# Kernel tuning notes

Hardware: AMD Instinct MI355X
Metric: run time of the kernel (lower is better)

Reference implementation:

```python
import jax, jax.numpy as jnp
import numpy as np

N, D = 8192, 128
BATCH_SIZE = 8192  # init kwarg; final loss divisor
EPS = 1e-12        # F.normalize eps


def _normalize(x):
    n = jnp.maximum(jnp.linalg.norm(x, axis=-1, keepdims=True), EPS)
    return x / n


def _alignment(x, y, alpha=2.0):
    # (x - y).norm(p=2, dim=1).pow(2).mean() == mean of squared row diffs
    return jnp.mean(jnp.sum((x - y) ** 2, axis=1))


def _uniformity(x, t=2.0):
    # torch.pdist(x).pow(2) == squared euclidean distance for all i<j pairs.
    # Use gram-matrix identity; mask to strict upper triangle.
    n = x.shape[0]
    sq = jnp.sum(x * x, axis=1)                      # [N]
    d2 = sq[:, None] + sq[None, :] - 2.0 * (x @ x.T)  # [N, N]
    d2 = jnp.maximum(d2, 0.0)
    iu = jnp.triu(jnp.ones((n, n), dtype=bool), k=1)
    num_pairs = n * (n - 1) // 2
    mean_val = jnp.sum(jnp.where(iu, jnp.exp(-t * d2), 0.0)) / num_pairs
    return jnp.log(mean_val)


def setup_inputs() -> dict:
    key = jax.random.key(0)
    k1, k2, k3 = jax.random.split(key, 3)
    return {
        "users": jax.random.normal(k1, (N, D), dtype=jnp.float32),
        "pos_items": jax.random.normal(k2, (N, D), dtype=jnp.float32),
        "neg_items": jax.random.normal(k3, (N, D), dtype=jnp.float32),
    }


def reference(users, pos_items, neg_items):
    # neg_items is accepted but unused, matching the original forward.
    user_n = _normalize(users)
    item_n = _normalize(pos_items)
    align = _alignment(user_n, item_n)
    uniform = 0.5 * (_uniformity(user_n) + _uniformity(item_n)) / 2.0
    loss = (align + uniform) / BATCH_SIZE
    return loss
```

## Files before the change

kernel.cpp:

```cpp
#include <hip/hip_runtime.h>
#include <hip/hip_bf16.h>

typedef int   i32x4  __attribute__((ext_vector_type(4)));
typedef int   i32x16 __attribute__((ext_vector_type(16)));

#define NROWS 8192
#define DIM   128
#define NB    64
#define JOBS_PER_MAT 2080

__device__ __forceinline__ float waveReduceSum(float v) {
    for (int off = 32; off; off >>= 1) v += __shfl_xor(v, off, 64);
    return v;
}

__device__ __forceinline__ float fast_exp2(float x) {
    return __builtin_amdgcn_exp2f(x);
}

__device__ __forceinline__ void gload16(const void* g, void* l) {
    __builtin_amdgcn_global_load_lds(
        (const __attribute__((address_space(1))) unsigned int*)(uintptr_t)g,
        (__attribute__((address_space(3))) unsigned int*)(uintptr_t)l,
        16, 0, 0);
}

__device__ __forceinline__ int tri(int b) { return b * NB - (b * (b - 1)) / 2; }

__global__ __launch_bounds__(256) void prep_kernel(
    const float* __restrict__ users, const float* __restrict__ pos,
    signed char* __restrict__ U8, signed char* __restrict__ P8,
    double* __restrict__ alignPart)
{
    const int tid  = threadIdx.x;
    const int lane = tid & 63;
    const int w    = tid >> 6;
    const int l32  = lane & 31;
    const int half = lane >> 5;
    const int r    = blockIdx.x * 8 + w * 2 + half;

    const float4 u4 = ((const float4*)users)[r * 32 + l32];
    const float4 p4 = ((const float4*)pos )[r * 32 + l32];

    float su = u4.x*u4.x + u4.y*u4.y + u4.z*u4.z + u4.w*u4.w;
    float sp = p4.x*p4.x + p4.y*p4.y + p4.z*p4.z + p4.w*p4.w;
    for (int off = 16; off; off >>= 1) {
        su += __shfl_xor(su, off, 64);
        sp += __shfl_xor(sp, off, 64);
    }
    const float nu  = fmaxf(sqrtf(su), 1e-12f);
    const float npp = fmaxf(sqrtf(sp), 1e-12f);

    const float ux = u4.x / nu,  uy = u4.y / nu,  uz = u4.z / nu,  uw = u4.w / nu;
    const float px = p4.x / npp, py = p4.y / npp, pz = p4.z / npp, pw = p4.w / npp;

    union { signed char c[4]; int i; } qu, qp;
    qu.c[0] = (signed char)__float2int_rn(ux * 127.0f);
    qu.c[1] = (signed char)__float2int_rn(uy * 127.0f);
    qu.c[2] = (signed char)__float2int_rn(uz * 127.0f);
    qu.c[3] = (signed char)__float2int_rn(uw * 127.0f);
    qp.c[0] = (signed char)__float2int_rn(px * 127.0f);
    qp.c[1] = (signed char)__float2int_rn(py * 127.0f);
    qp.c[2] = (signed char)__float2int_rn(pz * 127.0f);
    qp.c[3] = (signed char)__float2int_rn(pw * 127.0f);
    ((int*)U8)[r * 32 + l32] = qu.i;
    ((int*)P8)[r * 32 + l32] = qp.i;

    const float dx = ux - px, dy = uy - py, dz = uz - pz, dw = uw - pw;
    float al = dx*dx + dy*dy + dz*dz + dw*dw;
    for (int off = 16; off; off >>= 1) al += __shfl_xor(al, off, 64);
    al += __shfl_xor(al, 32, 64);

    __shared__ float wsum[4];
    if (lane == 0) wsum[w] = al;
    __syncthreads();
    if (tid == 0)
        alignPart[blockIdx.x] = (double)wsum[0] + (double)wsum[1]
                              + (double)wsum[2] + (double)wsum[3];
}

__global__ __launch_bounds__(256, 4) void gram_kernel(
    const signed char* __restrict__ U8, const signed char* __restrict__ P8,
    double* __restrict__ Spart)
{
    __shared__ __align__(16) unsigned char smem[32768];
    __shared__ float wsum[2][4];

    const int blk = blockIdx.x;
    const int j0  = blk * 2;
    const int mat = j0 >= JOBS_PER_MAT;
    const int t0  = j0 - (mat ? JOBS_PER_MAT : 0);

    int bi = (int)((NB + 0.5f) - sqrtf((NB + 0.5f) * (NB + 0.5f) - 2.0f * (float)t0));
    if (bi > 0 && tri(bi) > t0) --bi;
    if (tri(bi + 1) <= t0) ++bi;
    int bj = bi + (t0 - tri(bi));
    int bi1 = bi, bj1 = bj + 1;
    if (bj == NB - 1) { bi1 = bi + 1; bj1 = bi1; }

    const char* __restrict__ Xb = (const char*)(mat ? P8 : U8);

    const int tid  = threadIdx.x;
    const int lane = tid & 63;
    const int w    = tid >> 6;

    const int rl = lane >> 2;
    const int cg = (((lane & 3) ^ (rl & 3)) << 4);
    unsigned char* lbase = smem + w * 1024;

#define STAGE(p, h, tbi, tbj)                                               \
    {                                                                       \
        _Pragma("unroll")                                                   \
        for (int i_ = 0; i_ < 2; ++i_) {                                    \
            const int r_ = w * 16 + i_ * 64 + rl;                           \
            gload16(Xb + (size_t)((tbi) * 128 + r_) * 128 + (h) * 64 + cg,  \
                    lbase + (p) * 16384 + i_ * 4096);                       \
            gload16(Xb + (size_t)((tbj) * 128 + r_) * 128 + (h) * 64 + cg,  \
                    lbase + (p) * 16384 + 8192 + i_ * 4096);                \
        }                                                                   \
    }

    const int wm = w >> 1, wn = w & 1;
    const int l32 = lane & 31;
    const int lh  = lane >> 5;
    const unsigned cxor = (unsigned)(l32 & 3);
    const unsigned aRow0 = (unsigned)(wm * 64 + l32);
    const unsigned bRow0 = (unsigned)(wn * 64 + l32);

    i32x16 acc[2][2];
#define ZEROACC                                                             \
    _Pragma("unroll")                                                       \
    for (int mi_ = 0; mi_ < 2; ++mi_)                                       \
        _Pragma("unroll")                                                   \
        for (int ni_ = 0; ni_ < 2; ++ni_)                                   \
            _Pragma("unroll")                                               \
            for (int e_ = 0; e_ < 16; ++e_)                                 \
                acc[mi_][ni_][e_] = 0;
    ZEROACC

#define COMPUTE(p)                                                          \
    {                                                                       \
        const unsigned base = (p) * 16384;                                  \
        _Pragma("unroll")                                                   \
        for (int ks2 = 0; ks2 < 2; ++ks2) {                                 \
            const unsigned c = (((unsigned)(ks2 * 2 + lh)) ^ cxor) << 4;    \
            i32x4 a[2], b[2];                                               \
            _Pragma("unroll")                                               \
            for (int mi = 0; mi < 2; ++mi)                                  \
                a[mi] = *reinterpret_cast<const i32x4*>(                    \
                    smem + base + (aRow0 + mi * 32) * 64 + c);              \
            _Pragma("unroll")                                               \
            for (int ni = 0; ni < 2; ++ni)                                  \
                b[ni] = *reinterpret_cast<const i32x4*>(                    \
                    smem + base + 8192 + (bRow0 + ni * 32) * 64 + c);       \
            _Pragma("unroll")                                               \
            for (int mi = 0; mi < 2; ++mi)                                  \
                _Pragma("unroll")                                           \
                for (int ni = 0; ni < 2; ++ni)                              \
                    acc[mi][ni] = __builtin_amdgcn_mfma_i32_32x32x32_i8(    \
                        a[mi], b[ni], acc[mi][ni], 0, 0, 0);                \
        }                                                                   \
    }

    const float C1  = 4.0f * 1.4426950408889634f;
    const float C1s = C1 / 16129.0f;

#define EPILOGUE(slot)                                                      \
    {                                                                       \
        float s0 = 0.f, s1 = 0.f, s2 = 0.f, s3 = 0.f;                       \
        _Pragma("unroll")                                                   \
        for (int mi = 0; mi < 2; ++mi)                                      \
            _Pragma("unroll")                                               \
            for (int ni = 0; ni < 2; ++ni) {                                \
                const i32x16 v = acc[mi][ni];                               \
                _Pragma("unroll")                                           \
                for (int e = 0; e < 16; e += 4) {                           \
                    s0 += fast_exp2(fmaf((float)v[e + 0], C1s, -C1));       \
                    s1 += fast_exp2(fmaf((float)v[e + 1], C1s, -C1));       \
                    s2 += fast_exp2(fmaf((float)v[e + 2], C1s, -C1));       \
                    s3 += fast_exp2(fmaf((float)v[e + 3], C1s, -C1));       \
                }                                                           \
            }                                                               \
        const float s_ = waveReduceSum((s0 + s1) + (s2 + s3));              \
        if (lane == 0) wsum[slot][w] = s_;                                  \
    }

    STAGE(0, 0, bi, bj)
    __syncthreads();
    STAGE(1, 1, bi, bj)
    COMPUTE(0)
    __syncthreads();
    STAGE(0, 0, bi1, bj1)
    COMPUTE(1)
    EPILOGUE(0)
    ZEROACC
    __syncthreads();
    STAGE(1, 1, bi1, bj1)
    COMPUTE(0)
    if (tid == 0) {
        double bs = (double)wsum[0][0] + (double)wsum[0][1]
                  + (double)wsum[0][2] + (double)wsum[0][3];
        if (bi != bj) bs *= 2.0;
        Spart[j0] = bs;
    }
    __syncthreads();
    COMPUTE(1)
    EPILOGUE(1)
    __syncthreads();
    if (tid == 0) {
        double bs = (double)wsum[1][0] + (double)wsum[1][1]
                  + (double)wsum[1][2] + (double)wsum[1][3];
        if (bi1 != bj1) bs *= 2.0;
        Spart[j0 + 1] = bs;
    }
#undef STAGE
#undef COMPUTE
#undef ZEROACC
#undef EPILOGUE
}

__global__ __launch_bounds__(1024) void finalize_kernel(
    const double* __restrict__ alignPart, const double* __restrict__ Spart,
    float* __restrict__ out)
{
    const int tid = threadIdx.x;
    double a = 0.0, su = 0.0, sp = 0.0;
    for (int i = tid; i < 1024; i += 1024) a += alignPart[i];
    for (int i = tid; i < 2 * JOBS_PER_MAT; i += 1024) {
        const double v = Spart[i];
        if (i < JOBS_PER_MAT) su += v; else sp += v;
    }
    for (int off = 32; off; off >>= 1) {
        a  += __shfl_xor(a,  off, 64);
        su += __shfl_xor(su, off, 64);
        sp += __shfl_xor(sp, off, 64);
    }
    __shared__ double sh[3][16];
    const int lane = tid & 63, wid = tid >> 6;
    if (lane == 0) { sh[0][wid] = a; sh[1][wid] = su; sh[2][wid] = sp; }
    __syncthreads();
    if (tid == 0) {
        double A = 0.0, SU = 0.0, SP = 0.0;
        for (int i = 0; i < 16; ++i) { A += sh[0][i]; SU += sh[1][i]; SP += sh[2][i]; }
        const double Nd = 8192.0;
        const double npairs = Nd * (Nd - 1.0) * 0.5;
        const double align = A / Nd;
        const double mu = (SU - Nd) * 0.5 / npairs;
        const double mp = (SP - Nd) * 0.5 / npairs;
        const double uniform = 0.25 * (log(mu) + log(mp));
        out[0] = (float)((align + uniform) / 8192.0);
    }
}

extern "C" void kernel_launch(void* const* d_in, const int* in_sizes, int n_in,
                              void* d_out, int out_size, void* d_ws, size_t ws_size,
                              hipStream_t stream)
{
    const float* users = (const float*)d_in[0];
    const float* pos   = (const float*)d_in[1];
    float* out = (float*)d_out;

    char* ws = (char*)d_ws;
    signed char* U8 = (signed char*)ws;
    signed char* P8 = (signed char*)(ws + 1048576);
    double* alignPart = (double*)(ws + 2097152);
    double* Spart     = (double*)(ws + 2097152 + 8192);

    hipLaunchKernelGGL(prep_kernel, dim3(1024), dim3(256), 0, stream,
                       users, pos, U8, P8, alignPart);
    hipLaunchKernelGGL(gram_kernel, dim3(JOBS_PER_MAT), dim3(256), 0, stream,
                       U8, P8, Spart);
    hipLaunchKernelGGL(finalize_kernel, dim3(1), dim3(1024), 0, stream,
                       alignPart, Spart, out);
}
```

Before: 35.14 us.

## Process four gram tiles per block with full-K staging and double accumulators

Each gram block now handles four 128x128 tiles instead of two, staging the full 128-byte K dimension per tile into a 64KB double buffer rather than two 64-byte halves. Two accumulator sets alternate, so the exp epilogue of one tile overlaps the MFMA work of the next. The LDS swizzle widens to 8 chunks to match the 128-byte rows. The goal is fewer barriers and blocks and less per-tile epilogue exposure, paid for with double the shared memory, lower occupancy (launch bound 2) and more accumulator registers.

```diff
diff --git a/kernel.cpp b/kernel.cpp
--- a/kernel.cpp
+++ b/kernel.cpp
@@ -8,6 +8,7 @@
 #define DIM   128
 #define NB    64
 #define JOBS_PER_MAT 2080
+#define BLKS_PER_MAT 520
 
 __device__ __forceinline__ float waveReduceSum(float v) {
     for (int off = 32; off; off >>= 1) v += __shfl_xor(v, off, 64);
@@ -79,24 +80,29 @@
                               + (double)wsum[2] + (double)wsum[3];
 }
 
-__global__ __launch_bounds__(256, 4) void gram_kernel(
+__global__ __launch_bounds__(256, 2) void gram_kernel(
     const signed char* __restrict__ U8, const signed char* __restrict__ P8,
     double* __restrict__ Spart)
 {
-    __shared__ __align__(16) unsigned char smem[32768];
-    __shared__ float wsum[2][4];
+    __shared__ __align__(16) unsigned char smem[65536];
+    __shared__ float wsum[4][4];
 
     const int blk = blockIdx.x;
-    const int j0  = blk * 2;
-    const int mat = j0 >= JOBS_PER_MAT;
-    const int t0  = j0 - (mat ? JOBS_PER_MAT : 0);
+    const int mat = blk >= BLKS_PER_MAT;
+    const int t0  = (blk - (mat ? BLKS_PER_MAT : 0)) * 4;
 
     int bi = (int)((NB + 0.5f) - sqrtf((NB + 0.5f) * (NB + 0.5f) - 2.0f * (float)t0));
     if (bi > 0 && tri(bi) > t0) --bi;
     if (tri(bi + 1) <= t0) ++bi;
     int bj = bi + (t0 - tri(bi));
-    int bi1 = bi, bj1 = bj + 1;
-    if (bj == NB - 1) { bi1 = bi + 1; bj1 = bi1; }
+
+    int bis0 = bi, bjs0 = bj;
+    if (bj == NB - 1) { ++bi; bj = bi; } else ++bj;
+    int bis1 = bi, bjs1 = bj;
+    if (bj == NB - 1) { ++bi; bj = bi; } else ++bj;
+    int bis2 = bi, bjs2 = bj;
+    if (bj == NB - 1) { ++bi; bj = bi; } else ++bj;
+    int bis3 = bi, bjs3 = bj;
 
     const char* __restrict__ Xb = (const char*)(mat ? P8 : U8);
 
@@ -104,75 +110,74 @@
     const int lane = tid & 63;
     const int w    = tid >> 6;
 
-    const int rl = lane >> 2;
-    const int cg = (((lane & 3) ^ (rl & 3)) << 4);
-    unsigned char* lbase = smem + w * 1024;
-
-#define STAGE(p, h, tbi, tbj)                                               \
+    const int srow  = tid >> 3;
+    const int gcOff = (((tid & 7) ^ (srow & 7)) << 4);
+    unsigned char* lA0 = smem + w * 1024;
+
+#define STAGE(p, tbi, tbj)                                                  \
     {                                                                       \
         _Pragma("unroll")                                                   \
-        for (int i_ = 0; i_ < 2; ++i_) {                                    \
-            const int r_ = w * 16 + i_ * 64 + rl;                           \
-            gload16(Xb + (size_t)((tbi) * 128 + r_) * 128 + (h) * 64 + cg,  \
-                    lbase + (p) * 16384 + i_ * 4096);                       \
-            gload16(Xb + (size_t)((tbj) * 128 + r_) * 128 + (h) * 64 + cg,  \
-                    lbase + (p) * 16384 + 8192 + i_ * 4096);                \
+        for (int i_ = 0; i_ < 4; ++i_) {                                    \
+            gload16(Xb + (size_t)((tbi) * 128 + srow + 32 * i_) * 128 + gcOff, \
+                    lA0 + (p) * 32768 + i_ * 4096);                         \
+            gload16(Xb + (size_t)((tbj) * 128 + srow + 32 * i_) * 128 + gcOff, \
+                    lA0 + (p) * 32768 + 16384 + i_ * 4096);                 \
         }                                                                   \
     }
 
     const int wm = w >> 1, wn = w & 1;
     const int l32 = lane & 31;
     const int lh  = lane >> 5;
-    const unsigned cxor = (unsigned)(l32 & 3);
+    const unsigned cxor = (unsigned)(l32 & 7);
     const unsigned aRow0 = (unsigned)(wm * 64 + l32);
     const unsigned bRow0 = (unsigned)(wn * 64 + l32);
 
-    i32x16 acc[2][2];
-#define ZEROACC                                                             \
+    i32x16 accA[2][2], accB[2][2];
+
+#define ZERO(ACC)                                                           \
     _Pragma("unroll")                                                       \
     for (int mi_ = 0; mi_ < 2; ++mi_)                                       \
         _Pragma("unroll")                                                   \
         for (int ni_ = 0; ni_ < 2; ++ni_)                                   \
             _Pragma("unroll")                                               \
             for (int e_ = 0; e_ < 16; ++e_)                                 \
-                acc[mi_][ni_][e_] = 0;
-    ZEROACC
-
-#define COMPUTE(p)                                                          \
+                ACC[mi_][ni_][e_] = 0;
+
+#define COMPUTE(p, ACC)                                                     \
     {                                                                       \
-        const unsigned base = (p) * 16384;                                  \
-        _Pragma("unroll")                                                   \
-        for (int ks2 = 0; ks2 < 2; ++ks2) {                                 \
-            const unsigned c = (((unsigned)(ks2 * 2 + lh)) ^ cxor) << 4;    \
+        const unsigned base = (p) * 32768;                                  \
+        _Pragma("unroll")                                                   \
+        for (int ks = 0; ks < 4; ++ks) {                                    \
+            const unsigned c = (((unsigned)(ks * 2 + lh)) ^ cxor) << 4;     \
             i32x4 a[2], b[2];                                               \
             _Pragma("unroll")                                               \
             for (int mi = 0; mi < 2; ++mi)                                  \
                 a[mi] = *reinterpret_cast<const i32x4*>(                    \
-                    smem + base + (aRow0 + mi * 32) * 64 + c);              \
+                    smem + base + (aRow0 + mi * 32) * 128 + c);             \
             _Pragma("unroll")                                               \
             for (int ni = 0; ni < 2; ++ni)                                  \
                 b[ni] = *reinterpret_cast<const i32x4*>(                    \
-                    smem + base + 8192 + (bRow0 + ni * 32) * 64 + c);       \
+                    smem + base + 16384 + (bRow0 + ni * 32) * 128 + c);     \
             _Pragma("unroll")                                               \
             for (int mi = 0; mi < 2; ++mi)                                  \
                 _Pragma("unroll")                                           \
                 for (int ni = 0; ni < 2; ++ni)                              \
-                    acc[mi][ni] = __builtin_amdgcn_mfma_i32_32x32x32_i8(    \
-                        a[mi], b[ni], acc[mi][ni], 0, 0, 0);                \
+                    ACC[mi][ni] = __builtin_amdgcn_mfma_i32_32x32x32_i8(    \
+                        a[mi], b[ni], ACC[mi][ni], 0, 0, 0);                \
         }                                                                   \
     }
 
     const float C1  = 4.0f * 1.4426950408889634f;
     const float C1s = C1 / 16129.0f;
 
-#define EPILOGUE(slot)                                                      \
+#define EPI(ACC, slot)                                                      \
     {                                                                       \
         float s0 = 0.f, s1 = 0.f, s2 = 0.f, s3 = 0.f;                       \
         _Pragma("unroll")                                                   \
         for (int mi = 0; mi < 2; ++mi)                                      \
             _Pragma("unroll")                                               \
             for (int ni = 0; ni < 2; ++ni) {                                \
-                const i32x16 v = acc[mi][ni];                               \
+                const i32x16 v = ACC[mi][ni];                               \
                 _Pragma("unroll")                                           \
                 for (int e = 0; e < 16; e += 4) {                           \
                     s0 += fast_exp2(fmaf((float)v[e + 0], C1s, -C1));       \
@@ -185,38 +190,53 @@
         if (lane == 0) wsum[slot][w] = s_;                                  \
     }
 
-    STAGE(0, 0, bi, bj)
-    __syncthreads();
-    STAGE(1, 1, bi, bj)
-    COMPUTE(0)
-    __syncthreads();
-    STAGE(0, 0, bi1, bj1)
-    COMPUTE(1)
-    EPILOGUE(0)
-    ZEROACC
-    __syncthreads();
-    STAGE(1, 1, bi1, bj1)
-    COMPUTE(0)
+    ZERO(accA); ZERO(accB);
+    STAGE(0, bis0, bjs0)
+    __syncthreads();
+
+    STAGE(1, bis1, bjs1)
+    COMPUTE(0, accA)
+    __syncthreads();
+
+    STAGE(0, bis2, bjs2)
+    COMPUTE(1, accB)
+    EPI(accA, 0)
+    ZERO(accA);
+    __syncthreads();
+
+    STAGE(1, bis3, bjs3)
+    COMPUTE(0, accA)
+    EPI(accB, 1)
+    ZERO(accB);
+    __syncthreads();
+
+    COMPUTE(1, accB)
+    EPI(accA, 2)
+    EPI(accB, 3)
+    __syncthreads();
+
     if (tid == 0) {
-        double bs = (double)wsum[0][0] + (double)wsum[0][1]
+        double b0 = (double)wsum[0][0] + (double)wsum[0][1]
                   + (double)wsum[0][2] + (double)wsum[0][3];
-        if (bi != bj) bs *= 2.0;
-        Spart[j0] = bs;
-    }
-    __syncthreads();
-    COMPUTE(1)
-    EPILOGUE(1)
-    __syncthreads();
-    if (tid == 0) {
-        double bs = (double)wsum[1][0] + (double)wsum[1][1]
+        double b1 = (double)wsum[1][0] + (double)wsum[1][1]
                   + (double)wsum[1][2] + (double)wsum[1][3];
-        if (bi1 != bj1) bs *= 2.0;
-        Spart[j0 + 1] = bs;
+        double b2 = (double)wsum[2][0] + (double)wsum[2][1]
+                  + (double)wsum[2][2] + (double)wsum[2][3];
+        double b3 = (double)wsum[3][0] + (double)wsum[3][1]
+                  + (double)wsum[3][2] + (double)wsum[3][3];
+        if (bis0 != bjs0) b0 *= 2.0;
+        if (bis1 != bjs1) b1 *= 2.0;
+        if (bis2 != bjs2) b2 *= 2.0;
+        if (bis3 != bjs3) b3 *= 2.0;
+        Spart[blk * 4 + 0] = b0;
+        Spart[blk * 4 + 1] = b1;
+        Spart[blk * 4 + 2] = b2;
+        Spart[blk * 4 + 3] = b3;
     }
 #undef STAGE
 #undef COMPUTE
-#undef ZEROACC
-#undef EPILOGUE
+#undef ZERO
+#undef EPI
 }
 
 __global__ __launch_bounds__(1024) void finalize_kernel(
@@ -268,7 +288,7 @@
 
     hipLaunchKernelGGL(prep_kernel, dim3(1024), dim3(256), 0, stream,
                        users, pos, U8, P8, alignPart);
-    hipLaunchKernelGGL(gram_kernel, dim3(JOBS_PER_MAT), dim3(256), 0, stream,
+    hipLaunchKernelGGL(gram_kernel, dim3(2 * BLKS_PER_MAT), dim3(256), 0, stream,
                        U8, P8, Spart);
     hipLaunchKernelGGL(finalize_kernel, dim3(1), dim3(1024), 0, stream,
                        alignPart, Spart, out);
```

Result: slower. 37.19 us (+5.8%).
